# Kernel optimization log

Hardware: AMD Instinct MI355X
Metric: run time of the kernel (lower is better)

The kernel has to match this reference:

```python
import jax, jax.numpy as jnp
import numpy as np

EMBED_DIM = 512
Q_DIM = 64
V_DIM = 64
WINDOW_SIZE = 128
B, N = 2, 4096


def setup_inputs() -> dict:
    key = jax.random.key(0)
    ks = jax.random.split(key, 7)
    s = 1.0 / np.sqrt(EMBED_DIM)
    u = lambda k, shape: jax.random.uniform(k, shape, jnp.float32, -s, s)
    return {
        "x": jax.random.normal(ks[0], (B, N, EMBED_DIM), jnp.float32),
        "Wq": u(ks[1], (EMBED_DIM, Q_DIM)),
        "bq": u(ks[2], (Q_DIM,)),
        "Wk": u(ks[3], (EMBED_DIM, Q_DIM)),
        "bk": u(ks[4], (Q_DIM,)),
        "Wv": u(ks[5], (EMBED_DIM, V_DIM)),
        "bv": u(ks[6], (V_DIM,)),
    }


def reference(x, Wq, bq, Wk, bk, Wv, bv):
    b, n, _ = x.shape
    w = WINDOW_SIZE // 2
    Q = x @ Wq + bq  # (b, n, Qd)
    K = x @ Wk + bk  # (b, n, Qd)
    V = x @ Wv + bv  # (b, n, Vd)

    diags = jnp.arange(-w, w + 1)            # (nd,) offsets di
    nd = diags.shape[0]
    # Gather K[i + di] via padded K; invalid positions masked to 0 afterwards.
    Kpad = jnp.pad(K, ((0, 0), (w, w), (0, 0)))
    j = jnp.arange(n)[:, None] + diags[None, :]          # (n, nd) = i + di
    Kg = Kpad[:, j + w, :]                               # (b, n, nd, Qd)
    scores = jnp.einsum('bnd,bnod->bno', Q, Kg)          # (b, n, nd)
    valid = (j >= 0) & (j < n)
    scores = jnp.where(valid[None], scores, 0.0)

    # Faithful to original: diagonal dot products are scattered into the FIRST
    # nd columns of a dense (b, n, n) matrix (rest zeros), softmax over the
    # full n columns, then dense matmul with V.
    columns = jnp.zeros((b, n, n), dtype=x.dtype).at[:, :, :nd].set(scores)
    attn = jax.nn.softmax(columns, axis=2)               # (b, n, n)
    return attn @ V                                      # (b, n, Vd)
```

## Files before the change

### kernel.cpp

```cpp
#include <hip/hip_runtime.h>

typedef _Float16 half8 __attribute__((ext_vector_type(8)));
typedef float f32x4 __attribute__((ext_vector_type(4)));

#define NN 4096
#define NE 512
#define HD 64
#define KROWS 4288
#define KOFF  64
#define WSCALE (1.0f / 256.0f)

__device__ __forceinline__ void f16_split(float f, _Float16& hi, _Float16& lo) {
    hi = (_Float16)f;
    lo = (_Float16)(f - (float)hi);
}

#define MFMA16(a, b, c) __builtin_amdgcn_mfma_f32_16x16x32_f16((a), (b), (c), 0, 0, 0)

__global__ __launch_bounds__(256) void prep_kernel(
    const float* __restrict__ x,
    const float* __restrict__ Wq, const float* __restrict__ Wk,
    const float* __restrict__ Wv,
    _Float16* __restrict__ Wf, _Float16* __restrict__ Khi,
    _Float16* __restrict__ Vf, float* __restrict__ Vs,
    _Float16* __restrict__ Xfhi, _Float16* __restrict__ Xflo)
{
    const int blk = blockIdx.x;
    if (blk < 48) {
        const int gtid = blk * 256 + threadIdx.x;
        const int L = gtid & 63;
        {
            const int nt = (gtid >> 6) % 12;
            const int kt = gtid / 768;
            const int n = nt * 16 + (L & 15);
            const int kbase = kt * 32 + (L >> 4) * 8;
            const float* src; int col;
            if (n < 64)       { src = Wq; col = n; }
            else if (n < 128) { src = Wk; col = n - 64; }
            else              { src = Wv; col = n - 128; }
            half8 sh;
#pragma unroll
            for (int j = 0; j < 8; ++j)
                sh[j] = (_Float16)src[(size_t)(kbase + j) * HD + col];
            *(half8*)(Wf + (size_t)gtid * 8) = sh;
        }
        if (gtid < 6144) {
            const int p = gtid >> 3, o = gtid & 7;
            const int b = p / 192, q = p - b * 192;
            const size_t row = (size_t)b * KROWS + (q < 64 ? q : 4096 + q);
            const half8 z = {0, 0, 0, 0, 0, 0, 0, 0};
            *(half8*)(Khi + row * HD + o * 8) = z;
        }
        if (gtid < 3200) {
            const int rem = gtid % 1600;
            const int jt = rem / 320;
            const int nt = (rem / 64) % 5;
            half8 sh = {0, 0, 0, 0, 0, 0, 0, 0};
            if (nt == 4 && (L & 15) == 0) {
#pragma unroll
                for (int jj = 0; jj < 8; ++jj) {
                    const int j = jt * 32 + (L >> 4) * 8 + jj;
                    if (j < 129) sh[jj] = (_Float16)1.0f;
                }
            }
            *(half8*)(Vf + (size_t)gtid * 8) = sh;
        }
        if (gtid < 128) Vs[gtid] = 0.f;
    } else {
        const int gt = (blk - 48) * 256 + threadIdx.x;
#pragma unroll
        for (int i = 0; i < 4; ++i) {
            const int s = gt + i * 131072;
            const int rt = s >> 10;
            const int kt = (s >> 6) & 15;
            const int L = s & 63;
            const int row = rt * 16 + (L & 15);
            const int k = kt * 32 + (L >> 4) * 8;
            const float4 x0 = *(const float4*)(x + (size_t)row * NE + k);
            const float4 x1 = *(const float4*)(x + (size_t)row * NE + k + 4);
            const float xv[8] = {x0.x, x0.y, x0.z, x0.w,
                                 x1.x, x1.y, x1.z, x1.w};
            half8 hh, ll;
#pragma unroll
            for (int j = 0; j < 8; ++j) {
                _Float16 h, l; f16_split(xv[j], h, l);
                hh[j] = h; ll[j] = l;
            }
            *(half8*)(Xfhi + (size_t)s * 8) = hh;
            *(half8*)(Xflo + (size_t)s * 8) = ll;
        }
    }
}

__global__ __launch_bounds__(256) void proj_kernel(
    const _Float16* __restrict__ Xfhi, const _Float16* __restrict__ Xflo,
    const _Float16* __restrict__ Wf,
    const float* __restrict__ bq, const float* __restrict__ bk,
    const float* __restrict__ bv,
    _Float16* __restrict__ Qhi, _Float16* __restrict__ Qlo,
    _Float16* __restrict__ Khi, _Float16* __restrict__ Vf,
    float* __restrict__ Vs)
{
    __shared__ float V_lds[16][68];
    const int tid = threadIdx.x;
    const int L = tid & 63;
    const int w = tid >> 6;
    const int m = L & 15, kg = L >> 4;
    const int blk = blockIdx.x;
    const int r0 = blk * 16;
    const int b = blk >> 8;

    f32x4 acc[3];
#pragma unroll
    for (int t = 0; t < 3; ++t) acc[t] = (f32x4){0.f, 0.f, 0.f, 0.f};

    const _Float16* xf = Xfhi + ((size_t)blk * 16 * 64 + L) * 8;
    const _Float16* xl = Xflo + ((size_t)blk * 16 * 64 + L) * 8;
    const _Float16* wf = Wf + ((size_t)(w * 3) * 64 + L) * 8;

#pragma unroll
    for (int kt = 0; kt < 16; ++kt) {
        const half8 ahi = *(const half8*)(xf + (size_t)kt * 512);
        const half8 alo = *(const half8*)(xl + (size_t)kt * 512);
#pragma unroll
        for (int t = 0; t < 3; ++t) {
            const half8 wv = *(const half8*)(wf + ((size_t)kt * 12 + t) * 512);
            acc[t] = MFMA16(ahi, wv, acc[t]);
            acc[t] = MFMA16(alo, wv, acc[t]);
        }
    }

#pragma unroll
    for (int t = 0; t < 3; ++t) {
        const int nt = w * 3 + t;
        const int cgc = nt * 16 + m;
        const float bias = (cgc < 64) ? bq[cgc]
                         : (cgc < 128) ? bk[cgc - 64] : bv[cgc - 128];
#pragma unroll
        for (int r = 0; r < 4; ++r) {
            const int gr = r0 + kg * 4 + r;
            const float val = acc[t][r] + bias;
            if (cgc < 64) {
                _Float16 hh, ll; f16_split(val, hh, ll);
                Qhi[(size_t)gr * HD + cgc] = hh;
                Qlo[(size_t)gr * HD + cgc] = ll;
            } else if (cgc < 128) {
                const int d = cgc - 64, n = gr & 4095;
                Khi[((size_t)b * KROWS + KOFF + n) * HD + d] = (_Float16)val;
            } else {
                V_lds[kg * 4 + r][cgc - 128] = val;
            }
        }
    }
    __syncthreads();

    if (tid < 64) {
        float s = 0.f;
#pragma unroll
        for (int r = 0; r < 16; ++r) s += V_lds[r][tid];
        atomicAdd(&Vs[b * HD + tid], s);
    }

    {
        const int local = blk & 255;
        if (local < 8) {
            const int jt = local >> 1;
            if ((kg >> 1) == (local & 1)) {
                const int nt = w;
                half8 sh;
#pragma unroll
                for (int jj = 0; jj < 8; ++jj) {
                    const int lrow = (kg - (local & 1) * 2) * 8 + jj;
                    sh[jj] = (_Float16)V_lds[lrow][nt * 16 + m];
                }
                const size_t fo = ((size_t)((b * 25 + jt * 5 + nt) * 64 + L)) * 8;
                *(half8*)(Vf + fo) = sh;
            }
        } else if (local == 8 && kg == 0) {
            const int nt = w;
            half8 sh = {0, 0, 0, 0, 0, 0, 0, 0};
            sh[0] = (_Float16)V_lds[0][nt * 16 + m];
            const size_t fo = ((size_t)((b * 25 + 4 * 5 + nt) * 64 + L)) * 8;
            *(half8*)(Vf + fo) = sh;
        }
    }
}

__global__ __launch_bounds__(256) void attn_kernel(
    const _Float16* __restrict__ Qhi, const _Float16* __restrict__ Qlo,
    const _Float16* __restrict__ Khi, const _Float16* __restrict__ Vf,
    const float* __restrict__ Vs, float* __restrict__ out)
{
    __shared__ __align__(16) _Float16 wt_hi[16 * 168];
    __shared__ __align__(16) _Float16 wt_lo[16 * 168];
    __shared__ float den_lds[16];

    const int tid = threadIdx.x;
    const int L = tid & 63;
    const int w = tid >> 6;
    const int m = L & 15, kg = L >> 4;
    const int b = blockIdx.x >> 8;
    const int n0 = (blockIdx.x & 255) * 16;

    const _Float16* qp  = Qhi + ((size_t)(b * NN + n0 + m)) * HD + kg * 8;
    const _Float16* qp2 = Qlo + ((size_t)(b * NN + n0 + m)) * HD + kg * 8;
    const half8 qhi0 = *(const half8*)(qp);
    const half8 qhi1 = *(const half8*)(qp + 32);
    const half8 qlo0 = *(const half8*)(qp2);
    const half8 qlo1 = *(const half8*)(qp2 + 32);

    int kts[3]; int nkt;
    if (w == 3) { kts[0] = 3; kts[1] = 7; kts[2] = 8; nkt = 3; }
    else        { kts[0] = w; kts[1] = w + 4; kts[2] = 0; nkt = 2; }

    const _Float16* KB = Khi + (size_t)b * KROWS * HD;
    half8 kh0[3], kh1[3];
#pragma unroll
    for (int i = 0; i < 3; ++i) {
        if (i < nkt) {
            const _Float16* kp = KB + (size_t)(n0 + kts[i] * 16 + m) * HD + kg * 8;
            kh0[i] = *(const half8*)(kp);
            kh1[i] = *(const half8*)(kp + 32);
        }
    }

    half8 vhi[5], vh4[5];
#pragma unroll
    for (int jt = 0; jt < 5; ++jt) {
        const size_t fo = ((size_t)((b * 25 + jt * 5 + w) * 64 + L)) * 8;
        vhi[jt] = *(const half8*)(Vf + fo);
    }
    if (w == 0) {
#pragma unroll
        for (int jt = 0; jt < 5; ++jt) {
            const size_t fo4 = ((size_t)((b * 25 + jt * 5 + 4) * 64 + L)) * 8;
            vh4[jt] = *(const half8*)(Vf + fo4);
        }
    }

    for (int i = tid; i < (16 * 168) / 2; i += 256) {
        ((int*)wt_hi)[i] = 0;
        ((int*)wt_lo)[i] = 0;
    }
    __syncthreads();

#pragma unroll
    for (int i = 0; i < 3; ++i) {
        if (i < nkt) {
            f32x4 acc = (f32x4){0.f, 0.f, 0.f, 0.f};
            acc = MFMA16(qhi0, kh0[i], acc);
            acc = MFMA16(qhi1, kh1[i], acc);
            acc = MFMA16(qlo0, kh0[i], acc);
            acc = MFMA16(qlo1, kh1[i], acc);
            const int l = kts[i] * 16 + m;
#pragma unroll
            for (int r = 0; r < 4; ++r) {
                const int q = kg * 4 + r;
                const int j = l - q;
                if (j >= 0 && j < 129) {
                    const float wval = (__expf(acc[r]) - 1.0f) * WSCALE;
                    _Float16 hh, ll; f16_split(wval, hh, ll);
                    wt_hi[q * 168 + j] = hh;
                    wt_lo[q * 168 + j] = ll;
                }
            }
        }
    }
    __syncthreads();

    f32x4 oacc = (f32x4){0.f, 0.f, 0.f, 0.f};
    f32x4 dacc = (f32x4){0.f, 0.f, 0.f, 0.f};
#pragma unroll
    for (int jt = 0; jt < 5; ++jt) {
        const half8 whi = *(const half8*)(wt_hi + m * 168 + jt * 32 + kg * 8);
        const half8 wlo = *(const half8*)(wt_lo + m * 168 + jt * 32 + kg * 8);
        oacc = MFMA16(whi, vhi[jt], oacc);
        oacc = MFMA16(wlo, vhi[jt], oacc);
        if (w == 0) {
            dacc = MFMA16(whi, vh4[jt], dacc);
            dacc = MFMA16(wlo, vh4[jt], dacc);
        }
    }
    if (w == 0 && m == 0) {
#pragma unroll
        for (int r = 0; r < 4; ++r) den_lds[kg * 4 + r] = dacc[r];
    }
    __syncthreads();

    {
        const float vs = Vs[b * HD + w * 16 + m];
#pragma unroll
        for (int r = 0; r < 4; ++r) {
            const int q = kg * 4 + r;
            const float val = (vs + 256.0f * oacc[r])
                            / (4096.f + 256.0f * den_lds[q]);
            out[((size_t)(b * NN + n0 + q)) * HD + w * 16 + m] = val;
        }
    }
}

extern "C" void kernel_launch(void* const* d_in, const int* in_sizes, int n_in,
                              void* d_out, int out_size, void* d_ws, size_t ws_size,
                              hipStream_t stream)
{
    const float* x  = (const float*)d_in[0];
    const float* Wq = (const float*)d_in[1];
    const float* bq = (const float*)d_in[2];
    const float* Wk = (const float*)d_in[3];
    const float* bk = (const float*)d_in[4];
    const float* Wv = (const float*)d_in[5];
    const float* bv = (const float*)d_in[6];
    float* out = (float*)d_out;

    char* ws = (char*)d_ws;
    float*     Vs   = (float*)(ws + 0);
    _Float16*  Khi  = (_Float16*)(ws + 512);
    _Float16*  Qhi  = (_Float16*)(ws + 1098240);
    _Float16*  Qlo  = (_Float16*)(ws + 2146816);
    _Float16*  Wf   = (_Float16*)(ws + 3195392);
    _Float16*  Vf   = (_Float16*)(ws + 3392000);
    _Float16*  Xfhi = (_Float16*)(ws + 3443200);
    _Float16*  Xflo = (_Float16*)(ws + 11831808);

    prep_kernel<<<560, 256, 0, stream>>>(x, Wq, Wk, Wv, Wf, Khi, Vf, Vs,
                                         Xfhi, Xflo);
    proj_kernel<<<512, 256, 0, stream>>>(Xfhi, Xflo, Wf, bq, bk, bv,
                                         Qhi, Qlo, Khi, Vf, Vs);
    attn_kernel<<<512, 256, 0, stream>>>(Qhi, Qlo, Khi, Vf, Vs, out);
}
```

Measured before the change: 99.43 us.

## Fuse Q/K projection into attention kernel and compute V column sums from x sums

Replaces the separate projection kernel with a fused attention kernel. Each block recomputes its 16 Q rows and 160 neighbouring K rows with MFMA into LDS, so Q and K are never written to global memory. The V column sum is now taken algebraically from per-batch sums of x times Wv, so the full V projection and its atomics go away. Only the first V tile rows are projected, in a small prepB kernel. The cost is about ten times redundant K projection work per block, plus an extra strided reduction pass over x.

Result: slower. 150.6 us (+51.5%).

```diff
diff --git a/kernel.cpp b/kernel.cpp
--- a/kernel.cpp
+++ b/kernel.cpp
@@ -6,8 +6,6 @@
 #define NN 4096
 #define NE 512
 #define HD 64
-#define KROWS 4288
-#define KOFF  64
 #define WSCALE (1.0f / 256.0f)
 
 __device__ __forceinline__ void f16_split(float f, _Float16& hi, _Float16& lo) {
@@ -17,56 +15,32 @@
 
 #define MFMA16(a, b, c) __builtin_amdgcn_mfma_f32_16x16x32_f16((a), (b), (c), 0, 0, 0)
 
-__global__ __launch_bounds__(256) void prep_kernel(
+__global__ __launch_bounds__(256) void prepA_kernel(
     const float* __restrict__ x,
     const float* __restrict__ Wq, const float* __restrict__ Wk,
     const float* __restrict__ Wv,
-    _Float16* __restrict__ Wf, _Float16* __restrict__ Khi,
-    _Float16* __restrict__ Vf, float* __restrict__ Vs,
-    _Float16* __restrict__ Xfhi, _Float16* __restrict__ Xflo)
+    _Float16* __restrict__ Wf,
+    _Float16* __restrict__ Xfhi, _Float16* __restrict__ Xflo,
+    float* __restrict__ xpart)
 {
     const int blk = blockIdx.x;
     if (blk < 48) {
         const int gtid = blk * 256 + threadIdx.x;
         const int L = gtid & 63;
-        {
-            const int nt = (gtid >> 6) % 12;
-            const int kt = gtid / 768;
-            const int n = nt * 16 + (L & 15);
-            const int kbase = kt * 32 + (L >> 4) * 8;
-            const float* src; int col;
-            if (n < 64)       { src = Wq; col = n; }
-            else if (n < 128) { src = Wk; col = n - 64; }
-            else              { src = Wv; col = n - 128; }
-            half8 sh;
-#pragma unroll
-            for (int j = 0; j < 8; ++j)
-                sh[j] = (_Float16)src[(size_t)(kbase + j) * HD + col];
-            *(half8*)(Wf + (size_t)gtid * 8) = sh;
-        }
-        if (gtid < 6144) {
-            const int p = gtid >> 3, o = gtid & 7;
-            const int b = p / 192, q = p - b * 192;
-            const size_t row = (size_t)b * KROWS + (q < 64 ? q : 4096 + q);
-            const half8 z = {0, 0, 0, 0, 0, 0, 0, 0};
-            *(half8*)(Khi + row * HD + o * 8) = z;
-        }
-        if (gtid < 3200) {
-            const int rem = gtid % 1600;
-            const int jt = rem / 320;
-            const int nt = (rem / 64) % 5;
-            half8 sh = {0, 0, 0, 0, 0, 0, 0, 0};
-            if (nt == 4 && (L & 15) == 0) {
-#pragma unroll
-                for (int jj = 0; jj < 8; ++jj) {
-                    const int j = jt * 32 + (L >> 4) * 8 + jj;
-                    if (j < 129) sh[jj] = (_Float16)1.0f;
-                }
-            }
-            *(half8*)(Vf + (size_t)gtid * 8) = sh;
-        }
-        if (gtid < 128) Vs[gtid] = 0.f;
-    } else {
+        const int nt = (gtid >> 6) % 12;
+        const int kt = gtid / 768;
+        const int n = nt * 16 + (L & 15);
+        const int kbase = kt * 32 + (L >> 4) * 8;
+        const float* src; int col;
+        if (n < 64)       { src = Wq; col = n; }
+        else if (n < 128) { src = Wk; col = n - 64; }
+        else              { src = Wv; col = n - 128; }
+        half8 sh;
+#pragma unroll
+        for (int j = 0; j < 8; ++j)
+            sh[j] = (_Float16)src[(size_t)(kbase + j) * HD + col];
+        *(half8*)(Wf + (size_t)gtid * 8) = sh;
+    } else if (blk < 560) {
         const int gt = (blk - 48) * 256 + threadIdx.x;
 #pragma unroll
         for (int i = 0; i < 4; ++i) {
@@ -89,111 +63,107 @@
             *(half8*)(Xfhi + (size_t)s * 8) = hh;
             *(half8*)(Xflo + (size_t)s * 8) = ll;
         }
-    }
-}
-
-__global__ __launch_bounds__(256) void proj_kernel(
+    } else {
+        const int i = blk - 560;
+        const int b = i >> 5, seg = i & 31;
+        const int t = threadIdx.x;
+        const float* xb = x + ((size_t)b * NN + seg * 128) * NE + 2 * t;
+        float s0 = 0.f, s1 = 0.f;
+#pragma unroll 8
+        for (int r = 0; r < 128; ++r) {
+            const float2 v = *(const float2*)(xb + (size_t)r * NE);
+            s0 += v.x; s1 += v.y;
+        }
+        xpart[(size_t)i * 512 + 2 * t]     = s0;
+        xpart[(size_t)i * 512 + 2 * t + 1] = s1;
+    }
+}
+
+__global__ __launch_bounds__(256) void prepB_kernel(
+    const _Float16* __restrict__ Xfhi, const _Float16* __restrict__ Xflo,
+    const _Float16* __restrict__ Wf, const float* __restrict__ bv,
+    const float* __restrict__ xpart,
+    _Float16* __restrict__ Vf, float* __restrict__ xsum)
+{
+    const int blk = blockIdx.x;
+    const int tid = threadIdx.x;
+    if (blk < 18) {
+        __shared__ float V_lds[16][68];
+        const int b = blk / 9, rt = blk % 9;
+        const int L = tid & 63, w = tid >> 6;
+        const int m = L & 15, kg = L >> 4;
+        const int rtg = b * 256 + rt;
+        f32x4 acc = (f32x4){0.f, 0.f, 0.f, 0.f};
+#pragma unroll
+        for (int kt = 0; kt < 16; ++kt) {
+            const size_t ao = (((size_t)rtg * 16 + kt) * 64 + L) * 8;
+            const half8 ahi = *(const half8*)(Xfhi + ao);
+            const half8 alo = *(const half8*)(Xflo + ao);
+            const half8 wv = *(const half8*)(Wf + (((size_t)kt * 12 + 8 + w) * 64 + L) * 8);
+            acc = MFMA16(ahi, wv, acc);
+            acc = MFMA16(alo, wv, acc);
+        }
+        const float bvd = bv[w * 16 + m];
+#pragma unroll
+        for (int r = 0; r < 4; ++r)
+            V_lds[kg * 4 + r][w * 16 + m] = acc[r] + bvd;
+        __syncthreads();
+        if (rt < 8) {
+            const int jt = rt >> 1;
+            if ((kg >> 1) == (rt & 1)) {
+                const int nt = w;
+                half8 sh;
+#pragma unroll
+                for (int jj = 0; jj < 8; ++jj)
+                    sh[jj] = (_Float16)V_lds[(kg - (rt & 1) * 2) * 8 + jj][nt * 16 + m];
+                *(half8*)(Vf + ((size_t)((b * 25 + jt * 5 + nt) * 64 + L)) * 8) = sh;
+            }
+        } else {
+            const int nt = w;
+            half8 sh = {0, 0, 0, 0, 0, 0, 0, 0};
+            if (kg == 0) sh[0] = (_Float16)V_lds[0][nt * 16 + m];
+            *(half8*)(Vf + ((size_t)((b * 25 + 4 * 5 + nt) * 64 + L)) * 8) = sh;
+        }
+    } else if (blk < 20) {
+        const int b = blk - 18;
+        const int L = tid & 63;
+        for (int jt = tid >> 6; jt < 5; jt += 4) {
+            half8 sh = {0, 0, 0, 0, 0, 0, 0, 0};
+            if ((L & 15) == 0) {
+#pragma unroll
+                for (int jj = 0; jj < 8; ++jj) {
+                    const int j = jt * 32 + (L >> 4) * 8 + jj;
+                    if (j < 129) sh[jj] = (_Float16)1.0f;
+                }
+            }
+            *(half8*)(Vf + ((size_t)((b * 25 + jt * 5 + 4) * 64 + L)) * 8) = sh;
+        }
+    } else {
+        for (int o = tid; o < 1024; o += 256) {
+            const int b = o >> 9, k = o & 511;
+            float s = 0.f;
+#pragma unroll 8
+            for (int seg = 0; seg < 32; ++seg)
+                s += xpart[(size_t)(b * 32 + seg) * 512 + k];
+            xsum[o] = s;
+        }
+    }
+}
+
+__global__ __launch_bounds__(256) void fused_kernel(
     const _Float16* __restrict__ Xfhi, const _Float16* __restrict__ Xflo,
     const _Float16* __restrict__ Wf,
     const float* __restrict__ bq, const float* __restrict__ bk,
-    const float* __restrict__ bv,
-    _Float16* __restrict__ Qhi, _Float16* __restrict__ Qlo,
-    _Float16* __restrict__ Khi, _Float16* __restrict__ Vf,
-    float* __restrict__ Vs)
+    const float* __restrict__ Wv, const float* __restrict__ bv,
+    const float* __restrict__ xsum, const _Float16* __restrict__ Vf,
+    float* __restrict__ out)
 {
-    __shared__ float V_lds[16][68];
-    const int tid = threadIdx.x;
-    const int L = tid & 63;
-    const int w = tid >> 6;
-    const int m = L & 15, kg = L >> 4;
-    const int blk = blockIdx.x;
-    const int r0 = blk * 16;
-    const int b = blk >> 8;
-
-    f32x4 acc[3];
-#pragma unroll
-    for (int t = 0; t < 3; ++t) acc[t] = (f32x4){0.f, 0.f, 0.f, 0.f};
-
-    const _Float16* xf = Xfhi + ((size_t)blk * 16 * 64 + L) * 8;
-    const _Float16* xl = Xflo + ((size_t)blk * 16 * 64 + L) * 8;
-    const _Float16* wf = Wf + ((size_t)(w * 3) * 64 + L) * 8;
-
-#pragma unroll
-    for (int kt = 0; kt < 16; ++kt) {
-        const half8 ahi = *(const half8*)(xf + (size_t)kt * 512);
-        const half8 alo = *(const half8*)(xl + (size_t)kt * 512);
-#pragma unroll
-        for (int t = 0; t < 3; ++t) {
-            const half8 wv = *(const half8*)(wf + ((size_t)kt * 12 + t) * 512);
-            acc[t] = MFMA16(ahi, wv, acc[t]);
-            acc[t] = MFMA16(alo, wv, acc[t]);
-        }
-    }
-
-#pragma unroll
-    for (int t = 0; t < 3; ++t) {
-        const int nt = w * 3 + t;
-        const int cgc = nt * 16 + m;
-        const float bias = (cgc < 64) ? bq[cgc]
-                         : (cgc < 128) ? bk[cgc - 64] : bv[cgc - 128];
-#pragma unroll
-        for (int r = 0; r < 4; ++r) {
-            const int gr = r0 + kg * 4 + r;
-            const float val = acc[t][r] + bias;
-            if (cgc < 64) {
-                _Float16 hh, ll; f16_split(val, hh, ll);
-                Qhi[(size_t)gr * HD + cgc] = hh;
-                Qlo[(size_t)gr * HD + cgc] = ll;
-            } else if (cgc < 128) {
-                const int d = cgc - 64, n = gr & 4095;
-                Khi[((size_t)b * KROWS + KOFF + n) * HD + d] = (_Float16)val;
-            } else {
-                V_lds[kg * 4 + r][cgc - 128] = val;
-            }
-        }
-    }
-    __syncthreads();
-
-    if (tid < 64) {
-        float s = 0.f;
-#pragma unroll
-        for (int r = 0; r < 16; ++r) s += V_lds[r][tid];
-        atomicAdd(&Vs[b * HD + tid], s);
-    }
-
-    {
-        const int local = blk & 255;
-        if (local < 8) {
-            const int jt = local >> 1;
-            if ((kg >> 1) == (local & 1)) {
-                const int nt = w;
-                half8 sh;
-#pragma unroll
-                for (int jj = 0; jj < 8; ++jj) {
-                    const int lrow = (kg - (local & 1) * 2) * 8 + jj;
-                    sh[jj] = (_Float16)V_lds[lrow][nt * 16 + m];
-                }
-                const size_t fo = ((size_t)((b * 25 + jt * 5 + nt) * 64 + L)) * 8;
-                *(half8*)(Vf + fo) = sh;
-            }
-        } else if (local == 8 && kg == 0) {
-            const int nt = w;
-            half8 sh = {0, 0, 0, 0, 0, 0, 0, 0};
-            sh[0] = (_Float16)V_lds[0][nt * 16 + m];
-            const size_t fo = ((size_t)((b * 25 + 4 * 5 + nt) * 64 + L)) * 8;
-            *(half8*)(Vf + fo) = sh;
-        }
-    }
-}
-
-__global__ __launch_bounds__(256) void attn_kernel(
-    const _Float16* __restrict__ Qhi, const _Float16* __restrict__ Qlo,
-    const _Float16* __restrict__ Khi, const _Float16* __restrict__ Vf,
-    const float* __restrict__ Vs, float* __restrict__ out)
-{
+    __shared__ __align__(16) _Float16 K_lds[160][72];
+    __shared__ float Q_lds[16][68];
     __shared__ __align__(16) _Float16 wt_hi[16 * 168];
     __shared__ __align__(16) _Float16 wt_lo[16 * 168];
     __shared__ float den_lds[16];
+    __shared__ float vs_lds[4][64];
 
     const int tid = threadIdx.x;
     const int L = tid & 63;
@@ -201,28 +171,7 @@
     const int m = L & 15, kg = L >> 4;
     const int b = blockIdx.x >> 8;
     const int n0 = (blockIdx.x & 255) * 16;
-
-    const _Float16* qp  = Qhi + ((size_t)(b * NN + n0 + m)) * HD + kg * 8;
-    const _Float16* qp2 = Qlo + ((size_t)(b * NN + n0 + m)) * HD + kg * 8;
-    const half8 qhi0 = *(const half8*)(qp);
-    const half8 qhi1 = *(const half8*)(qp + 32);
-    const half8 qlo0 = *(const half8*)(qp2);
-    const half8 qlo1 = *(const half8*)(qp2 + 32);
-
-    int kts[3]; int nkt;
-    if (w == 3) { kts[0] = 3; kts[1] = 7; kts[2] = 8; nkt = 3; }
-    else        { kts[0] = w; kts[1] = w + 4; kts[2] = 0; nkt = 2; }
-
-    const _Float16* KB = Khi + (size_t)b * KROWS * HD;
-    half8 kh0[3], kh1[3];
-#pragma unroll
-    for (int i = 0; i < 3; ++i) {
-        if (i < nkt) {
-            const _Float16* kp = KB + (size_t)(n0 + kts[i] * 16 + m) * HD + kg * 8;
-            kh0[i] = *(const half8*)(kp);
-            kh1[i] = *(const half8*)(kp + 32);
-        }
-    }
+    const int rt0 = n0 >> 4;
 
     half8 vhi[5], vh4[5];
 #pragma unroll
@@ -242,26 +191,97 @@
         ((int*)wt_hi)[i] = 0;
         ((int*)wt_lo)[i] = 0;
     }
+
+    {
+        const float bkd = bk[w * 16 + m];
+        for (int rt = 0; rt < 10; ++rt) {
+            int lrt = rt0 - 4 + rt;
+            lrt = (lrt < 0) ? 0 : (lrt > 255 ? 255 : lrt);
+            const int rtg = b * 256 + lrt;
+            f32x4 acc = (f32x4){0.f, 0.f, 0.f, 0.f};
+#pragma unroll
+            for (int kt = 0; kt < 16; ++kt) {
+                const size_t ao = (((size_t)rtg * 16 + kt) * 64 + L) * 8;
+                const half8 ahi = *(const half8*)(Xfhi + ao);
+                const half8 alo = *(const half8*)(Xflo + ao);
+                const half8 wv = *(const half8*)(Wf + (((size_t)kt * 12 + 4 + w) * 64 + L) * 8);
+                acc = MFMA16(ahi, wv, acc);
+                acc = MFMA16(alo, wv, acc);
+            }
+#pragma unroll
+            for (int r = 0; r < 4; ++r)
+                K_lds[rt * 16 + kg * 4 + r][w * 16 + m] = (_Float16)(acc[r] + bkd);
+        }
+    }
+    {
+        const int rtg = b * 256 + rt0;
+        f32x4 acc = (f32x4){0.f, 0.f, 0.f, 0.f};
+#pragma unroll
+        for (int kt = 0; kt < 16; ++kt) {
+            const size_t ao = (((size_t)rtg * 16 + kt) * 64 + L) * 8;
+            const half8 ahi = *(const half8*)(Xfhi + ao);
+            const half8 alo = *(const half8*)(Xflo + ao);
+            const half8 wv = *(const half8*)(Wf + (((size_t)kt * 12 + w) * 64 + L) * 8);
+            acc = MFMA16(ahi, wv, acc);
+            acc = MFMA16(alo, wv, acc);
+        }
+        const float bqd = bq[w * 16 + m];
+#pragma unroll
+        for (int r = 0; r < 4; ++r)
+            Q_lds[kg * 4 + r][w * 16 + m] = acc[r] + bqd;
+    }
+    {
+        float s = (w == 0) ? 4096.0f * bv[L] : 0.0f;
+        const float* xs = xsum + b * 512 + w * 128;
+#pragma unroll 8
+        for (int k = 0; k < 128; ++k)
+            s += xs[k] * Wv[(size_t)(w * 128 + k) * HD + L];
+        vs_lds[w][L] = s;
+    }
     __syncthreads();
 
-#pragma unroll
-    for (int i = 0; i < 3; ++i) {
-        if (i < nkt) {
-            f32x4 acc = (f32x4){0.f, 0.f, 0.f, 0.f};
-            acc = MFMA16(qhi0, kh0[i], acc);
-            acc = MFMA16(qhi1, kh1[i], acc);
-            acc = MFMA16(qlo0, kh0[i], acc);
-            acc = MFMA16(qlo1, kh1[i], acc);
-            const int l = kts[i] * 16 + m;
-#pragma unroll
-            for (int r = 0; r < 4; ++r) {
-                const int q = kg * 4 + r;
-                const int j = l - q;
-                if (j >= 0 && j < 129) {
-                    const float wval = (__expf(acc[r]) - 1.0f) * WSCALE;
-                    _Float16 hh, ll; f16_split(wval, hh, ll);
-                    wt_hi[q * 168 + j] = hh;
-                    wt_lo[q * 168 + j] = ll;
+    {
+        const float4 qa0 = *(const float4*)(&Q_lds[m][kg * 8]);
+        const float4 qa1 = *(const float4*)(&Q_lds[m][kg * 8 + 4]);
+        const float4 qb0 = *(const float4*)(&Q_lds[m][32 + kg * 8]);
+        const float4 qb1 = *(const float4*)(&Q_lds[m][32 + kg * 8 + 4]);
+        const float q0v[8] = {qa0.x, qa0.y, qa0.z, qa0.w, qa1.x, qa1.y, qa1.z, qa1.w};
+        const float q1v[8] = {qb0.x, qb0.y, qb0.z, qb0.w, qb1.x, qb1.y, qb1.z, qb1.w};
+        half8 qhi0, qlo0, qhi1, qlo1;
+#pragma unroll
+        for (int j = 0; j < 8; ++j) {
+            _Float16 h, l;
+            f16_split(q0v[j], h, l); qhi0[j] = h; qlo0[j] = l;
+            f16_split(q1v[j], h, l); qhi1[j] = h; qlo1[j] = l;
+        }
+
+        const int nkt = (w < 2) ? 3 : 2;
+        const int kts[3] = {w, w + 4, w + 8};
+#pragma unroll
+        for (int i = 0; i < 3; ++i) {
+            if (i < nkt) {
+                const int kt = kts[i];
+                const half8 kh0 = *(const half8*)(&K_lds[kt * 16 + m][kg * 8]);
+                const half8 kh1 = *(const half8*)(&K_lds[kt * 16 + m][32 + kg * 8]);
+                f32x4 acc = (f32x4){0.f, 0.f, 0.f, 0.f};
+                acc = MFMA16(qhi0, kh0, acc);
+                acc = MFMA16(qhi1, kh1, acc);
+                acc = MFMA16(qlo0, kh0, acc);
+                acc = MFMA16(qlo1, kh1, acc);
+                const int l = kt * 16 + m;
+#pragma unroll
+                for (int r = 0; r < 4; ++r) {
+                    const int q = kg * 4 + r;
+                    const int j = l - q;
+                    if (j >= 0 && j < 129) {
+                        const int key = n0 - 64 + l;
+                        float wval = 0.f;
+                        if (key >= 0 && key < NN)
+                            wval = (__expf(acc[r]) - 1.0f) * WSCALE;
+                        _Float16 hh, ll; f16_split(wval, hh, ll);
+                        wt_hi[q * 168 + j] = hh;
+                        wt_lo[q * 168 + j] = ll;
+                    }
                 }
             }
         }
@@ -288,13 +308,14 @@
     __syncthreads();
 
     {
-        const float vs = Vs[b * HD + w * 16 + m];
+        const int d = w * 16 + m;
+        const float vs = vs_lds[0][d] + vs_lds[1][d] + vs_lds[2][d] + vs_lds[3][d];
 #pragma unroll
         for (int r = 0; r < 4; ++r) {
             const int q = kg * 4 + r;
             const float val = (vs + 256.0f * oacc[r])
                             / (4096.f + 256.0f * den_lds[q]);
-            out[((size_t)(b * NN + n0 + q)) * HD + w * 16 + m] = val;
+            out[((size_t)(b * NN + n0 + q)) * HD + d] = val;
         }
     }
 }
@@ -313,18 +334,15 @@
     float* out = (float*)d_out;
 
     char* ws = (char*)d_ws;
-    float*     Vs   = (float*)(ws + 0);
-    _Float16*  Khi  = (_Float16*)(ws + 512);
-    _Float16*  Qhi  = (_Float16*)(ws + 1098240);
-    _Float16*  Qlo  = (_Float16*)(ws + 2146816);
-    _Float16*  Wf   = (_Float16*)(ws + 3195392);
-    _Float16*  Vf   = (_Float16*)(ws + 3392000);
-    _Float16*  Xfhi = (_Float16*)(ws + 3443200);
-    _Float16*  Xflo = (_Float16*)(ws + 11831808);
-
-    prep_kernel<<<560, 256, 0, stream>>>(x, Wq, Wk, Wv, Wf, Khi, Vf, Vs,
-                                         Xfhi, Xflo);
-    proj_kernel<<<512, 256, 0, stream>>>(Xfhi, Xflo, Wf, bq, bk, bv,
-                                         Qhi, Qlo, Khi, Vf, Vs);
-    attn_kernel<<<512, 256, 0, stream>>>(Qhi, Qlo, Khi, Vf, Vs, out);
-}
+    _Float16* Wf    = (_Float16*)(ws + 0);
+    _Float16* Xfhi  = (_Float16*)(ws + 196608);
+    _Float16* Xflo  = (_Float16*)(ws + 8585216);
+    _Float16* Vf    = (_Float16*)(ws + 16973824);
+    float*    xpart = (float*)(ws + 17025024);
+    float*    xsum  = (float*)(ws + 17156096);
+
+    prepA_kernel<<<624, 256, 0, stream>>>(x, Wq, Wk, Wv, Wf, Xfhi, Xflo, xpart);
+    prepB_kernel<<<21, 256, 0, stream>>>(Xfhi, Xflo, Wf, bv, xpart, Vf, xsum);
+    fused_kernel<<<512, 256, 0, stream>>>(Xfhi, Xflo, Wf, bq, bk, Wv, bv,
+                                          xsum, Vf, out);
+}
```
